# Performance work log

Hardware: AMD Instinct MI355X
Metric: run time of the kernel (lower is better)

The kernel has to match this reference:

```python
import jax, jax.numpy as jnp
import numpy as np

B, C, F, HO, WO = 8, 3, 5, 256, 256


def setup_inputs() -> dict:
    key = jax.random.key(0)
    k1, k2, k3 = jax.random.split(key, 3)
    tensorInput = jax.random.normal(k1, (B, C, HO * F, WO * F), dtype=jnp.float32)
    tensorVertical = jax.random.normal(k2, (B, F, HO, WO), dtype=jnp.float32)
    tensorHorizontal = jax.random.normal(k3, (B, F, HO, WO), dtype=jnp.float32)
    return {
        "tensorInput": tensorInput,
        "tensorVertical": tensorVertical,
        "tensorHorizontal": tensorHorizontal,
    }


def reference(tensorInput, tensorVertical, tensorHorizontal):
    # input [B,C,Ho*F,Wo*F] -> disjoint FxF patches [B,C,Ho,F,Wo,F]
    b, c, h, w = tensorInput.shape
    f = tensorVertical.shape[1]
    ho, wo = h // f, w // f
    patches = tensorInput.reshape(b, c, ho, f, wo, f)
    # out[b,c,y,x] = sum_{i,j} patches[b,c,y,i,x,j] * V[b,i,y,x] * H[b,j,y,x]
    out = jnp.einsum(
        "bcyixj,biyx,bjyx->bcyx",
        patches,
        tensorVertical,
        tensorHorizontal,
    )
    return out
```

## Files before the change

kernel.cpp:

```cpp
#include <hip/hip_runtime.h>


#define Bsz 8
#define Csz 3
#define Fsz 5
#define HOsz 256
#define WOsz 256

__global__ __launch_bounds__(256) void sepconv_kernel(
    const float* __restrict__ in,
    const float* __restrict__ V,
    const float* __restrict__ Hh,
    float* __restrict__ out)
{
    const int idx = blockIdx.x * blockDim.x + threadIdx.x;
    const int x  = idx & (WOsz - 1);
    const int y  = (idx >> 8) & (HOsz - 1);
    const int bc = idx >> 16;
    if (bc >= Bsz * Csz) return;
    const int c = bc % Csz;
    const int b = bc / Csz;

    constexpr int W = WOsz * Fsz;
    constexpr int Hfull = HOsz * Fsz;
    constexpr int PLANE = HOsz * WOsz;

    const float* vp = V  + (b * Fsz * PLANE) + y * WOsz + x;
    const float* hp = Hh + (b * Fsz * PLANE) + y * WOsz + x;
    float v[Fsz], h[Fsz];
#pragma unroll
    for (int i = 0; i < Fsz; ++i) {
        v[i] = vp[i * PLANE];
        h[i] = hp[i * PLANE];
    }

    const float* ip = in + ((size_t)(b * Csz + c) * Hfull + y * Fsz) * W + x * Fsz;

    float acc = 0.f;
#pragma unroll
    for (int i = 0; i < Fsz; ++i) {
        float rs = 0.f;
#pragma unroll
        for (int j = 0; j < Fsz; ++j)
            rs = fmaf(ip[(size_t)i * W + j], h[j], rs);
        acc = fmaf(rs, v[i], acc);
    }
    out[idx] = acc;
}

extern "C" void kernel_launch(void* const* d_in, const int* in_sizes, int n_in,
                              void* d_out, int out_size, void* d_ws, size_t ws_size,
                              hipStream_t stream) {
    const float* in = (const float*)d_in[0];
    const float* V  = (const float*)d_in[1];
    const float* Hh = (const float*)d_in[2];
    float* out = (float*)d_out;

    const int total = Bsz * Csz * HOsz * WOsz;
    const int block = 256;
    const int grid = (total + block - 1) / block;
    sepconv_kernel<<<grid, block, 0, stream>>>(in, V, Hh, out);
}
```

Measured before the change: 231.9 us.

## Stage patch rows in shared memory via coalesced float4 loads

Each block now handles one output row and cooperatively loads the five contiguous input rows (6400 floats) into LDS with float4 loads, then each thread reads its 5x5 patch from shared memory. This replaces strided per-thread global loads, where each thread read five scattered 5-float chunks, with fully coalesced vector loads. It costs 25.6KB of LDS per block and a barrier, which may limit occupancy, and shared-memory reads at stride 5 can cause bank conflicts.

```diff
diff --git a/kernel.cpp b/kernel.cpp
--- a/kernel.cpp
+++ b/kernel.cpp
@@ -13,20 +13,30 @@
     const float* __restrict__ Hh,
     float* __restrict__ out)
 {
-    const int idx = blockIdx.x * blockDim.x + threadIdx.x;
-    const int x  = idx & (WOsz - 1);
-    const int y  = (idx >> 8) & (HOsz - 1);
-    const int bc = idx >> 16;
-    if (bc >= Bsz * Csz) return;
-    const int c = bc % Csz;
-    const int b = bc / Csz;
+    constexpr int W = WOsz * Fsz;
+    constexpr int PLANE = HOsz * WOsz;
+    constexpr int ROW_FLOATS = Fsz * W;
+    constexpr int NV4 = ROW_FLOATS / 4;
+    __shared__ float tile[ROW_FLOATS];
 
-    constexpr int W = WOsz * Fsz;
-    constexpr int Hfull = HOsz * Fsz;
-    constexpr int PLANE = HOsz * WOsz;
+    const int tid = threadIdx.x;
+    const int y   = blockIdx.x & (HOsz - 1);
+    const int bc  = blockIdx.x >> 8;
+    const int c   = bc % Csz;
+    const int b   = bc / Csz;
+    const int x   = tid;
 
-    const float* vp = V  + (b * Fsz * PLANE) + y * WOsz + x;
-    const float* hp = Hh + (b * Fsz * PLANE) + y * WOsz + x;
+    const float4* src = reinterpret_cast<const float4*>(
+        in + ((size_t)(b * Csz + c) * (HOsz * Fsz) + (size_t)y * Fsz) * W);
+    float4* dst = reinterpret_cast<float4*>(tile);
+#pragma unroll
+    for (int k = 0; k < 6; ++k)
+        dst[tid + k * 256] = src[tid + k * 256];
+    if (tid < NV4 - 6 * 256)
+        dst[tid + 6 * 256] = src[tid + 6 * 256];
+
+    const float* vp = V  + (size_t)b * Fsz * PLANE + y * WOsz + x;
+    const float* hp = Hh + (size_t)b * Fsz * PLANE + y * WOsz + x;
     float v[Fsz], h[Fsz];
 #pragma unroll
     for (int i = 0; i < Fsz; ++i) {
@@ -34,18 +44,21 @@
         h[i] = hp[i * PLANE];
     }
 
-    const float* ip = in + ((size_t)(b * Csz + c) * Hfull + y * Fsz) * W + x * Fsz;
+    __syncthreads();
 
     float acc = 0.f;
 #pragma unroll
     for (int i = 0; i < Fsz; ++i) {
-        float rs = 0.f;
-#pragma unroll
-        for (int j = 0; j < Fsz; ++j)
-            rs = fmaf(ip[(size_t)i * W + j], h[j], rs);
+        const float* r = tile + i * W + x * Fsz;
+        float rs = r[0] * h[0];
+        rs = fmaf(r[1], h[1], rs);
+        rs = fmaf(r[2], h[2], rs);
+        rs = fmaf(r[3], h[3], rs);
+        rs = fmaf(r[4], h[4], rs);
         acc = fmaf(rs, v[i], acc);
     }
-    out[idx] = acc;
+
+    out[((size_t)bc * HOsz + y) * WOsz + x] = acc;
 }
 
 extern "C" void kernel_launch(void* const* d_in, const int* in_sizes, int n_in,
@@ -56,8 +69,6 @@
     const float* Hh = (const float*)d_in[2];
     float* out = (float*)d_out;
 
-    const int total = Bsz * Csz * HOsz * WOsz;
-    const int block = 256;
-    const int grid = (total + block - 1) / block;
-    sepconv_kernel<<<grid, block, 0, stream>>>(in, V, Hh, out);
+    const int grid = Bsz * Csz * HOsz;
+    sepconv_kernel<<<grid, 256, 0, stream>>>(in, V, Hh, out);
 }
```

New measurement: 233.4 us. No clear change (+0.6%).
